# Kernel optimization log

Measured on AMD Instinct MI355X. Metric: run time of the kernel, lower is better.

Reference implementation:

```python
import jax, jax.numpy as jnp
import numpy as np

TOP_K = 8
N_EXPERTS = 64
ALPHA = 0.01

def setup_inputs() -> dict:
    key = jax.random.key(0)
    k1, k2 = jax.random.split(key)
    hidden_states = jax.random.normal(k1, (8, 4096, 1024), dtype=jnp.float32)
    weight = jax.random.normal(k2, (N_EXPERTS, 1024), dtype=jnp.float32) * 0.02
    return {"hidden_states": hidden_states, "weight": weight}

def reference(hidden_states, weight):
    bsz, seq_len, h = hidden_states.shape
    tokens = hidden_states.reshape(-1, h).astype(jnp.float32)          # [T, h]
    logits = tokens @ weight.astype(jnp.float32).T                     # [T, E]
    scores = jax.nn.softmax(logits, axis=-1)                           # [T, E]
    topk_weights, topk_indices = jax.lax.top_k(scores, TOP_K)          # [T, K]
    topk_indices = jnp.clip(topk_indices, 0, N_EXPERTS - 1)
    # renormalize top-k probabilities (norm_topk_prob=True, top_k>1)
    denom = topk_weights.sum(axis=-1, keepdims=True) + 1e-20
    topk_weights = topk_weights / denom
    # expert usage counts (bincount / scatter path)
    expert_counts = jnp.zeros((N_EXPERTS,), jnp.int32).at[topk_indices.reshape(-1)].add(1)
    # sequence aux loss (training path, seq_aux=True)
    idx_b = topk_indices.reshape(bsz, seq_len * TOP_K)                 # [B, S*K]
    ce = jnp.zeros((bsz, N_EXPERTS), jnp.float32)
    ce = ce.at[jnp.arange(bsz)[:, None], idx_b].add(1.0)
    ce = ce * (N_EXPERTS / (seq_len * TOP_K))
    scores_seq = scores.reshape(bsz, seq_len, N_EXPERTS)
    aux_loss = ((ce * scores_seq.mean(axis=1)).sum(axis=1)).mean() * ALPHA
    return (topk_indices.astype(jnp.int32),
            topk_weights.astype(hidden_states.dtype),
            aux_loss,
            expert_counts)
```

## Files before the change

kernel.cpp:

```cpp
#include <hip/hip_runtime.h>

#define NTOK 32768
#define HDIM 1024
#define NEXP 64
#define TK   8
#define NB   8
#define SEQ  4096

#define MB   64
#define KC   64
#define NCH  (HDIM / KC)
#define NTHR 512

typedef __attribute__((ext_vector_type(8))) short bf16x8;
typedef __attribute__((ext_vector_type(4))) float f32x4;

union BF8 { bf16x8 v; unsigned u[4]; };

__device__ inline unsigned f2bf(float x) {
    unsigned u = __float_as_uint(x);
    return (u + 0x7FFFu + ((u >> 16) & 1u)) >> 16;
}

__device__ inline void split4(float4 v, unsigned* hp, unsigned* lp) {
    unsigned h0 = f2bf(v.x), h1 = f2bf(v.y), h2 = f2bf(v.z), h3 = f2bf(v.w);
    unsigned l0 = f2bf(v.x - __uint_as_float(h0 << 16));
    unsigned l1 = f2bf(v.y - __uint_as_float(h1 << 16));
    unsigned l2 = f2bf(v.z - __uint_as_float(h2 << 16));
    unsigned l3 = f2bf(v.w - __uint_as_float(h3 << 16));
    hp[0] = h0 | (h1 << 16); hp[1] = h2 | (h3 << 16);
    lp[0] = l0 | (l1 << 16); lp[1] = l2 | (l3 << 16);
}

__device__ __forceinline__ void gl16(const void* g, void* l) {
    __builtin_amdgcn_global_load_lds(
        (const __attribute__((address_space(1))) void*)g,
        (__attribute__((address_space(3))) void*)l, 16, 0, 0);
}

__global__ void wsplit(const float* __restrict__ w,
                       unsigned short* __restrict__ whi,
                       unsigned short* __restrict__ wlo)
{
    int T = blockIdx.x * 256 + threadIdx.x;
    int slot = T >> 6, l = T & 63;
    int c = slot >> 3, s = (slot >> 2) & 1, n = slot & 3;
    int e = n * 16 + (l & 15);
    int k = c * 64 + s * 32 + (l >> 4) * 8;
    const float* src = w + (size_t)e * HDIM + k;
    float4 v0 = *(const float4*)(src);
    float4 v1 = *(const float4*)(src + 4);
    unsigned hp[4], lp[4];
    split4(v0, &hp[0], &lp[0]);
    split4(v1, &hp[2], &lp[2]);
    ((uint4*)whi)[T] = make_uint4(hp[0], hp[1], hp[2], hp[3]);
    ((uint4*)wlo)[T] = make_uint4(lp[0], lp[1], lp[2], lp[3]);
}

__global__ __launch_bounds__(NTHR, 4) void moe_main(
    const float* __restrict__ hidden,
    const unsigned short* __restrict__ w2hi,
    const unsigned short* __restrict__ w2lo,
    float* __restrict__ out,
    float* __restrict__ ws)
{
    __shared__ __align__(16) unsigned char smem[32768];
    float* sLog = (float*)smem;
    __shared__ float mxArr[MB];
    __shared__ float smSum[NEXP];
    __shared__ int   hist[NEXP];

    const int tid   = threadIdx.x;
    const int w     = tid >> 6;
    const int l     = tid & 63;
    const int m     = l & 15;
    const int q     = l >> 4;
    const int wm    = w >> 1;
    const int wn    = w & 1;
    const int t0    = blockIdx.x * MB;
    const int wbase = tid & 448;

    if (tid < NEXP) { smSum[tid] = 0.f; hist[tid] = 0; }

    f32x4 acc[2];
#pragma unroll
    for (int n = 0; n < 2; ++n) acc[n] = (f32x4)0.f;

#pragma unroll
    for (int i = 0; i < 2; ++i) {
        int slot = i * NTHR + tid;
        int r = slot >> 4, p = slot & 15, b = p ^ (r & 15);
        gl16(hidden + (size_t)(t0 + r) * HDIM + b * 4,
             smem + (size_t)(i * NTHR + wbase) * 16);
    }
    __syncthreads();

    for (int c = 0; c < NCH; ++c) {
        const unsigned char* Ab = smem + (c & 1) * 16384;

        bf16x8 bh[2][2], bl[2][2];
#pragma unroll
        for (int s = 0; s < 2; ++s)
#pragma unroll
            for (int n = 0; n < 2; ++n) {
                size_t off = ((size_t)(c * 8 + s * 4 + wn * 2 + n) * 64 + l) * 8;
                bh[s][n] = *(const bf16x8*)(w2hi + off);
                bl[s][n] = *(const bf16x8*)(w2lo + off);
            }

        if (c + 1 < NCH) {
            unsigned char* nb = smem + ((c + 1) & 1) * 16384;
            const int kc = (c + 1) * KC;
#pragma unroll
            for (int i = 0; i < 2; ++i) {
                int slot = i * NTHR + tid;
                int r = slot >> 4, p = slot & 15, b = p ^ (r & 15);
                gl16(hidden + (size_t)(t0 + r) * HDIM + kc + b * 4,
                     nb + (size_t)(i * NTHR + wbase) * 16);
            }
        }

#pragma unroll
        for (int s = 0; s < 2; ++s) {
            const int r  = wm * 16 + m;
            const int b0 = s * 8 + q * 2;
            const int p0 = b0 ^ m, p1 = (b0 + 1) ^ m;
            float4 a0 = *(const float4*)(Ab + ((size_t)r * 16 + p0) * 16);
            float4 a1 = *(const float4*)(Ab + ((size_t)r * 16 + p1) * 16);
            BF8 ah, al;
            split4(a0, &ah.u[0], &al.u[0]);
            split4(a1, &ah.u[2], &al.u[2]);
#pragma unroll
            for (int n = 0; n < 2; ++n) {
                acc[n] = __builtin_amdgcn_mfma_f32_16x16x32_bf16(ah.v, bh[s][n], acc[n], 0, 0, 0);
                acc[n] = __builtin_amdgcn_mfma_f32_16x16x32_bf16(al.v, bh[s][n], acc[n], 0, 0, 0);
                acc[n] = __builtin_amdgcn_mfma_f32_16x16x32_bf16(ah.v, bl[s][n], acc[n], 0, 0, 0);
            }
        }
        __syncthreads();
    }

#pragma unroll
    for (int n = 0; n < 2; ++n)
#pragma unroll
        for (int r = 0; r < 4; ++r)
            sLog[(wm * 16 + q * 4 + r) * 66 + (wn * 2 + n) * 16 + m] = acc[n][r];
    __syncthreads();

    float regSm = 0.f;
    for (int j = 0; j < 8; ++j) {
        int t = w * 8 + j;
        float x = sLog[t * 66 + l];
        float mx = x;
#pragma unroll
        for (int off = 32; off; off >>= 1) mx = fmaxf(mx, __shfl_xor(mx, off));
        float p = __expf(x - mx);
        float sd = p;
#pragma unroll
        for (int off = 32; off; off >>= 1) sd += __shfl_xor(sd, off);
        regSm += p / sd;
        if (l == 0) mxArr[t] = mx;
    }
    atomicAdd(&smSum[l], regSm);
    __syncthreads();

    if (w == 0) {
        const float mx = mxArr[l];
        unsigned long long s8[TK];
#pragma unroll
        for (int j = 0; j < TK; ++j) s8[j] = 0ull;
        for (int e = 0; e < NEXP; ++e) {
            float x = sLog[l * 66 + e];
            unsigned u = __float_as_uint(x);
            unsigned k32 = (u & 0x80000000u) ? ~u : (u | 0x80000000u);
            unsigned long long key = ((unsigned long long)k32 << 6)
                                   | (unsigned long long)(63 - e);
            if (key > s8[TK - 1]) {
#pragma unroll
                for (int j = 0; j < TK; ++j) {
                    unsigned long long hi = s8[j] > key ? s8[j] : key;
                    key = s8[j] > key ? key : s8[j];
                    s8[j] = hi;
                }
            }
        }
        float ev[TK]; int ei[TK]; float sum = 0.f;
#pragma unroll
        for (int j = 0; j < TK; ++j) {
            unsigned k32 = (unsigned)(s8[j] >> 6);
            unsigned u = (k32 >> 31) ? (k32 ^ 0x80000000u) : ~k32;
            ev[j] = __expf(__uint_as_float(u) - mx);
            sum += ev[j];
            ei[j] = 63 - (int)(s8[j] & 63ull);
        }
        int t = t0 + l;
        float4 i0 = make_float4((float)ei[0], (float)ei[1], (float)ei[2], (float)ei[3]);
        float4 i1 = make_float4((float)ei[4], (float)ei[5], (float)ei[6], (float)ei[7]);
        *(float4*)(out + (size_t)t * TK)     = i0;
        *(float4*)(out + (size_t)t * TK + 4) = i1;
        float rs = 1.f / (sum + 1e-20f);
        float4 w0 = make_float4(ev[0] * rs, ev[1] * rs, ev[2] * rs, ev[3] * rs);
        float4 w1 = make_float4(ev[4] * rs, ev[5] * rs, ev[6] * rs, ev[7] * rs);
        *(float4*)(out + (size_t)NTOK * TK + (size_t)t * TK)     = w0;
        *(float4*)(out + (size_t)NTOK * TK + (size_t)t * TK + 4) = w1;
#pragma unroll
        for (int j = 0; j < TK; ++j) atomicAdd(&hist[ei[j]], 1);
    }
    __syncthreads();

    if (tid < NEXP) {
        int b = blockIdx.x >> 6;
        atomicAdd(&ws[b * NEXP + tid], (float)hist[tid]);
        atomicAdd(&ws[NB * NEXP + b * NEXP + tid], smSum[tid]);
    }
}

__global__ void moe_finalize(const float* __restrict__ ws, float* __restrict__ out)
{
    int e = threadIdx.x;
    float cnt = 0.f, accv = 0.f;
#pragma unroll
    for (int b = 0; b < NB; ++b) {
        float c  = ws[b * NEXP + e];
        float sm = ws[NB * NEXP + b * NEXP + e];
        cnt += c;
        accv += c * sm;
    }
    out[(size_t)NTOK * TK * 2 + 1 + e] = cnt;
#pragma unroll
    for (int off = 32; off; off >>= 1) accv += __shfl_xor(accv, off);
    if (e == 0) {
        float aux = 0.01f * accv * ((float)NEXP / ((float)SEQ * (float)TK))
                    / (float)SEQ / (float)NB;
        out[(size_t)NTOK * TK * 2] = aux;
    }
}

extern "C" void kernel_launch(void* const* d_in, const int* in_sizes, int n_in,
                              void* d_out, int out_size, void* d_ws, size_t ws_size,
                              hipStream_t stream)
{
    const float* hidden = (const float*)d_in[0];
    const float* weight = (const float*)d_in[1];
    float* out  = (float*)d_out;
    float* wsf  = (float*)d_ws;
    unsigned short* w2hi = (unsigned short*)(wsf + 2 * NB * NEXP);
    unsigned short* w2lo = w2hi + NEXP * HDIM;

    hipMemsetAsync(d_ws, 0, 2 * NB * NEXP * sizeof(float), stream);
    wsplit<<<32, 256, 0, stream>>>(weight, w2hi, w2lo);
    moe_main<<<NTOK / MB, NTHR, 0, stream>>>(hidden, w2hi, w2lo, out, wsf);
    moe_finalize<<<1, 64, 0, stream>>>(wsf, out);
}
```

Baseline: 231.8 us.

## Restructure GEMM into 16-token full-K tiles with double-buffered LDS prefetch

Each block now handles 128 tokens as 8 sequential 16-token tiles. Every tile loads the full 1024-wide hidden rows (64KB) into double-buffered LDS, and each of 4 waves computes 16 experts over the whole K dimension. Softmax and top-k run per tile, spread across waves. The goal is to overlap the next tile's load with the current tile's compute and cut per-chunk synchronisation. The cost is 128KB of LDS per block, which limits occupancy to about one block per CU. Weight fragments are also reloaded from global memory for every tile.

```diff
diff --git a/kernel.cpp b/kernel.cpp
--- a/kernel.cpp
+++ b/kernel.cpp
@@ -7,10 +7,13 @@
 #define NB   8
 #define SEQ  4096
 
-#define MB   64
-#define KC   64
-#define NCH  (HDIM / KC)
-#define NTHR 512
+#define TPB   128
+#define TT    16
+#define NTILE (TPB / TT)
+#define NTHR  256
+#define NBLK  (NTOK / TPB)
+
+#define ABUF  65536
 
 typedef __attribute__((ext_vector_type(8))) short bf16x8;
 typedef __attribute__((ext_vector_type(4))) float f32x4;
@@ -57,16 +60,15 @@
     ((uint4*)wlo)[T] = make_uint4(lp[0], lp[1], lp[2], lp[3]);
 }
 
-__global__ __launch_bounds__(NTHR, 4) void moe_main(
+__global__ __launch_bounds__(NTHR, 1) void moe_main(
     const float* __restrict__ hidden,
     const unsigned short* __restrict__ w2hi,
     const unsigned short* __restrict__ w2lo,
     float* __restrict__ out,
     float* __restrict__ ws)
 {
-    __shared__ __align__(16) unsigned char smem[32768];
-    float* sLog = (float*)smem;
-    __shared__ float mxArr[MB];
+    __shared__ __align__(16) unsigned char smem[2 * ABUF];
+    __shared__ float sLog[TT * 66];
     __shared__ float smSum[NEXP];
     __shared__ int   hist[NEXP];
 
@@ -75,141 +77,135 @@
     const int l     = tid & 63;
     const int m     = l & 15;
     const int q     = l >> 4;
-    const int wm    = w >> 1;
-    const int wn    = w & 1;
-    const int t0    = blockIdx.x * MB;
-    const int wbase = tid & 448;
+    const int wbase = tid & 192;
+    const size_t t0 = (size_t)blockIdx.x * TPB;
 
     if (tid < NEXP) { smSum[tid] = 0.f; hist[tid] = 0; }
 
-    f32x4 acc[2];
-#pragma unroll
-    for (int n = 0; n < 2; ++n) acc[n] = (f32x4)0.f;
-
-#pragma unroll
-    for (int i = 0; i < 2; ++i) {
-        int slot = i * NTHR + tid;
-        int r = slot >> 4, p = slot & 15, b = p ^ (r & 15);
-        gl16(hidden + (size_t)(t0 + r) * HDIM + b * 4,
-             smem + (size_t)(i * NTHR + wbase) * 16);
+    {
+        const float* base = hidden + t0 * HDIM;
+#pragma unroll
+        for (int i = 0; i < 16; ++i) {
+            int L = i * NTHR + tid;
+            int r = L >> 8;
+            int u = L & 255;
+            int sc = (u & 0xF0) | ((u & 15) ^ r);
+            gl16(base + (size_t)r * HDIM + sc * 4,
+                 smem + (size_t)(i * NTHR + wbase) * 16);
+        }
     }
     __syncthreads();
 
-    for (int c = 0; c < NCH; ++c) {
-        const unsigned char* Ab = smem + (c & 1) * 16384;
-
-        bf16x8 bh[2][2], bl[2][2];
-#pragma unroll
-        for (int s = 0; s < 2; ++s)
-#pragma unroll
-            for (int n = 0; n < 2; ++n) {
-                size_t off = ((size_t)(c * 8 + s * 4 + wn * 2 + n) * 64 + l) * 8;
-                bh[s][n] = *(const bf16x8*)(w2hi + off);
-                bl[s][n] = *(const bf16x8*)(w2lo + off);
-            }
-
-        if (c + 1 < NCH) {
-            unsigned char* nb = smem + ((c + 1) & 1) * 16384;
-            const int kc = (c + 1) * KC;
-#pragma unroll
-            for (int i = 0; i < 2; ++i) {
-                int slot = i * NTHR + tid;
-                int r = slot >> 4, p = slot & 15, b = p ^ (r & 15);
-                gl16(hidden + (size_t)(t0 + r) * HDIM + kc + b * 4,
+    float mxKeep = 0.f;
+
+    for (int tile = 0; tile < NTILE; ++tile) {
+        const unsigned char* Ab = smem + (tile & 1) * ABUF;
+
+        if (tile + 1 < NTILE) {
+            unsigned char* nb = smem + ((tile + 1) & 1) * ABUF;
+            const float* base = hidden + (t0 + (size_t)(tile + 1) * TT) * HDIM;
+#pragma unroll
+            for (int i = 0; i < 16; ++i) {
+                int L = i * NTHR + tid;
+                int r = L >> 8;
+                int u = L & 255;
+                int sc = (u & 0xF0) | ((u & 15) ^ r);
+                gl16(base + (size_t)r * HDIM + sc * 4,
                      nb + (size_t)(i * NTHR + wbase) * 16);
             }
         }
 
-#pragma unroll
-        for (int s = 0; s < 2; ++s) {
-            const int r  = wm * 16 + m;
-            const int b0 = s * 8 + q * 2;
-            const int p0 = b0 ^ m, p1 = (b0 + 1) ^ m;
-            float4 a0 = *(const float4*)(Ab + ((size_t)r * 16 + p0) * 16);
-            float4 a1 = *(const float4*)(Ab + ((size_t)r * 16 + p1) * 16);
+        f32x4 acc = (f32x4)0.f;
+#pragma unroll
+        for (int s = 0; s < 32; ++s) {
+            size_t boff = ((size_t)((s >> 1) * 8 + (s & 1) * 4 + w) * 64 + l) * 8;
+            bf16x8 bh = *(const bf16x8*)(w2hi + boff);
+            bf16x8 bl = *(const bf16x8*)(w2lo + boff);
+            int grp = (s >> 1) << 4;
+            int p0  = ((s & 1) * 8 + q * 2)     ^ m;
+            int p1  = ((s & 1) * 8 + q * 2 + 1) ^ m;
+            float4 a0 = *(const float4*)(Ab + ((size_t)(m << 8) + grp + p0) * 16);
+            float4 a1 = *(const float4*)(Ab + ((size_t)(m << 8) + grp + p1) * 16);
             BF8 ah, al;
             split4(a0, &ah.u[0], &al.u[0]);
             split4(a1, &ah.u[2], &al.u[2]);
-#pragma unroll
-            for (int n = 0; n < 2; ++n) {
-                acc[n] = __builtin_amdgcn_mfma_f32_16x16x32_bf16(ah.v, bh[s][n], acc[n], 0, 0, 0);
-                acc[n] = __builtin_amdgcn_mfma_f32_16x16x32_bf16(al.v, bh[s][n], acc[n], 0, 0, 0);
-                acc[n] = __builtin_amdgcn_mfma_f32_16x16x32_bf16(ah.v, bl[s][n], acc[n], 0, 0, 0);
-            }
-        }
+            acc = __builtin_amdgcn_mfma_f32_16x16x32_bf16(ah.v, bh, acc, 0, 0, 0);
+            acc = __builtin_amdgcn_mfma_f32_16x16x32_bf16(al.v, bh, acc, 0, 0, 0);
+            acc = __builtin_amdgcn_mfma_f32_16x16x32_bf16(ah.v, bl, acc, 0, 0, 0);
+        }
+
         __syncthreads();
-    }
-
-#pragma unroll
-    for (int n = 0; n < 2; ++n)
-#pragma unroll
-        for (int r = 0; r < 4; ++r)
-            sLog[(wm * 16 + q * 4 + r) * 66 + (wn * 2 + n) * 16 + m] = acc[n][r];
-    __syncthreads();
-
-    float regSm = 0.f;
-    for (int j = 0; j < 8; ++j) {
-        int t = w * 8 + j;
-        float x = sLog[t * 66 + l];
-        float mx = x;
-#pragma unroll
-        for (int off = 32; off; off >>= 1) mx = fmaxf(mx, __shfl_xor(mx, off));
-        float p = __expf(x - mx);
-        float sd = p;
-#pragma unroll
-        for (int off = 32; off; off >>= 1) sd += __shfl_xor(sd, off);
-        regSm += p / sd;
-        if (l == 0) mxArr[t] = mx;
-    }
-    atomicAdd(&smSum[l], regSm);
-    __syncthreads();
-
-    if (w == 0) {
-        const float mx = mxArr[l];
-        unsigned long long s8[TK];
-#pragma unroll
-        for (int j = 0; j < TK; ++j) s8[j] = 0ull;
-        for (int e = 0; e < NEXP; ++e) {
-            float x = sLog[l * 66 + e];
-            unsigned u = __float_as_uint(x);
-            unsigned k32 = (u & 0x80000000u) ? ~u : (u | 0x80000000u);
-            unsigned long long key = ((unsigned long long)k32 << 6)
-                                   | (unsigned long long)(63 - e);
-            if (key > s8[TK - 1]) {
-#pragma unroll
-                for (int j = 0; j < TK; ++j) {
-                    unsigned long long hi = s8[j] > key ? s8[j] : key;
-                    key = s8[j] > key ? key : s8[j];
-                    s8[j] = hi;
+
+#pragma unroll
+        for (int rr = 0; rr < 4; ++rr)
+            sLog[(q * 4 + rr) * 66 + w * 16 + m] = acc[rr];
+        __syncthreads();
+
+        float regSm = 0.f;
+#pragma unroll
+        for (int jj = 0; jj < 4; ++jj) {
+            int t = w * 4 + jj;
+            float x = sLog[t * 66 + l];
+            float mx = x;
+#pragma unroll
+            for (int off = 32; off; off >>= 1) mx = fmaxf(mx, __shfl_xor(mx, off));
+            float p = __expf(x - mx);
+            float sd = p;
+#pragma unroll
+            for (int off = 32; off; off >>= 1) sd += __shfl_xor(sd, off);
+            regSm += p / sd;
+            if (jj == (l & 3)) mxKeep = mx;
+        }
+        atomicAdd(&smSum[l], regSm);
+
+        if (l < 4) {
+            const int   tl = w * 4 + l;
+            const float mx = mxKeep;
+            unsigned long long s8[TK];
+#pragma unroll
+            for (int j = 0; j < TK; ++j) s8[j] = 0ull;
+            for (int e = 0; e < NEXP; ++e) {
+                float x = sLog[tl * 66 + e];
+                unsigned u = __float_as_uint(x);
+                unsigned k32 = (u & 0x80000000u) ? ~u : (u | 0x80000000u);
+                unsigned long long key = ((unsigned long long)k32 << 6)
+                                       | (unsigned long long)(63 - e);
+                if (key > s8[TK - 1]) {
+#pragma unroll
+                    for (int j = 0; j < TK; ++j) {
+                        unsigned long long hi = s8[j] > key ? s8[j] : key;
+                        key = s8[j] > key ? key : s8[j];
+                        s8[j] = hi;
+                    }
                 }
             }
-        }
-        float ev[TK]; int ei[TK]; float sum = 0.f;
-#pragma unroll
-        for (int j = 0; j < TK; ++j) {
-            unsigned k32 = (unsigned)(s8[j] >> 6);
-            unsigned u = (k32 >> 31) ? (k32 ^ 0x80000000u) : ~k32;
-            ev[j] = __expf(__uint_as_float(u) - mx);
-            sum += ev[j];
-            ei[j] = 63 - (int)(s8[j] & 63ull);
-        }
-        int t = t0 + l;
-        float4 i0 = make_float4((float)ei[0], (float)ei[1], (float)ei[2], (float)ei[3]);
-        float4 i1 = make_float4((float)ei[4], (float)ei[5], (float)ei[6], (float)ei[7]);
-        *(float4*)(out + (size_t)t * TK)     = i0;
-        *(float4*)(out + (size_t)t * TK + 4) = i1;
-        float rs = 1.f / (sum + 1e-20f);
-        float4 w0 = make_float4(ev[0] * rs, ev[1] * rs, ev[2] * rs, ev[3] * rs);
-        float4 w1 = make_float4(ev[4] * rs, ev[5] * rs, ev[6] * rs, ev[7] * rs);
-        *(float4*)(out + (size_t)NTOK * TK + (size_t)t * TK)     = w0;
-        *(float4*)(out + (size_t)NTOK * TK + (size_t)t * TK + 4) = w1;
-#pragma unroll
-        for (int j = 0; j < TK; ++j) atomicAdd(&hist[ei[j]], 1);
+            float ev[TK]; int ei[TK]; float sum = 0.f;
+#pragma unroll
+            for (int j = 0; j < TK; ++j) {
+                unsigned k32 = (unsigned)(s8[j] >> 6);
+                unsigned u = (k32 >> 31) ? (k32 ^ 0x80000000u) : ~k32;
+                ev[j] = __expf(__uint_as_float(u) - mx);
+                sum += ev[j];
+                ei[j] = 63 - (int)(s8[j] & 63ull);
+            }
+            size_t t = t0 + (size_t)tile * TT + tl;
+            float4 i0 = make_float4((float)ei[0], (float)ei[1], (float)ei[2], (float)ei[3]);
+            float4 i1 = make_float4((float)ei[4], (float)ei[5], (float)ei[6], (float)ei[7]);
+            *(float4*)(out + t * TK)     = i0;
+            *(float4*)(out + t * TK + 4) = i1;
+            float rs = 1.f / (sum + 1e-20f);
+            float4 w0 = make_float4(ev[0] * rs, ev[1] * rs, ev[2] * rs, ev[3] * rs);
+            float4 w1 = make_float4(ev[4] * rs, ev[5] * rs, ev[6] * rs, ev[7] * rs);
+            *(float4*)(out + (size_t)NTOK * TK + t * TK)     = w0;
+            *(float4*)(out + (size_t)NTOK * TK + t * TK + 4) = w1;
+#pragma unroll
+            for (int j = 0; j < TK; ++j) atomicAdd(&hist[ei[j]], 1);
+        }
     }
     __syncthreads();
 
     if (tid < NEXP) {
-        int b = blockIdx.x >> 6;
+        int b = blockIdx.x >> 5;
         atomicAdd(&ws[b * NEXP + tid], (float)hist[tid]);
         atomicAdd(&ws[NB * NEXP + b * NEXP + tid], smSum[tid]);
     }
@@ -249,6 +245,6 @@
 
     hipMemsetAsync(d_ws, 0, 2 * NB * NEXP * sizeof(float), stream);
     wsplit<<<32, 256, 0, stream>>>(weight, w2hi, w2lo);
-    moe_main<<<NTOK / MB, NTHR, 0, stream>>>(hidden, w2hi, w2lo, out, wsf);
+    moe_main<<<NBLK, NTHR, 0, stream>>>(hidden, w2hi, w2lo, out, wsf);
     moe_finalize<<<1, 64, 0, stream>>>(wsf, out);
 }
```

New measurement: 399.7 us. 1.72x slower.

## Split GEMM from gating and add 5-deep async ring buffer for hidden and weights

Applied to the files above, without the earlier changes.

Splits the fused kernel into a GEMM kernel that writes logits to workspace and a separate gating kernel for softmax, top-k and aux stats. The GEMM now uses 128-token tiles with K-chunks of 32, stages both the hidden-state slice and the weight hi/lo slices through a 5-slot LDS ring with prefetch three chunks ahead, and waits with explicit vmcnt counts instead of a full __syncthreads per chunk. The goal is to hide global-load latency on the memory-bound hidden-state stream and to reuse the weight fragments across two M sub-tiles. In exchange the logits make an extra round trip through global memory, there is one more kernel launch, and occupancy drops because of the larger LDS footprint.

```diff
diff --git a/kernel.cpp b/kernel.cpp
--- a/kernel.cpp
+++ b/kernel.cpp
@@ -7,10 +7,16 @@
 #define NB   8
 #define SEQ  4096
 
-#define MB   64
-#define KC   64
-#define NCH  (HDIM / KC)
-#define NTHR 512
+#define MB    128
+#define KC    32
+#define NCH   (HDIM / KC)
+#define NTHR  512
+#define NBLK  (NTOK / MB)
+
+#define RING  5
+#define CH_A  16384
+#define CH_B  4096
+#define CHSZ  (CH_A + 2 * CH_B)
 
 typedef __attribute__((ext_vector_type(8))) short bf16x8;
 typedef __attribute__((ext_vector_type(4))) float f32x4;
@@ -57,18 +63,13 @@
     ((uint4*)wlo)[T] = make_uint4(lp[0], lp[1], lp[2], lp[3]);
 }
 
-__global__ __launch_bounds__(NTHR, 4) void moe_main(
+__global__ __launch_bounds__(NTHR, 2) void moe_gemm(
     const float* __restrict__ hidden,
     const unsigned short* __restrict__ w2hi,
     const unsigned short* __restrict__ w2lo,
-    float* __restrict__ out,
-    float* __restrict__ ws)
-{
-    __shared__ __align__(16) unsigned char smem[32768];
-    float* sLog = (float*)smem;
-    __shared__ float mxArr[MB];
-    __shared__ float smSum[NEXP];
-    __shared__ int   hist[NEXP];
+    float* __restrict__ logits)
+{
+    __shared__ __align__(16) unsigned char smem[RING * CHSZ];
 
     const int tid   = threadIdx.x;
     const int w     = tid >> 6;
@@ -77,76 +78,118 @@
     const int q     = l >> 4;
     const int wm    = w >> 1;
     const int wn    = w & 1;
-    const int t0    = blockIdx.x * MB;
     const int wbase = tid & 448;
-
-    if (tid < NEXP) { smSum[tid] = 0.f; hist[tid] = 0; }
-
-    f32x4 acc[2];
-#pragma unroll
-    for (int n = 0; n < 2; ++n) acc[n] = (f32x4)0.f;
-
-#pragma unroll
-    for (int i = 0; i < 2; ++i) {
-        int slot = i * NTHR + tid;
-        int r = slot >> 4, p = slot & 15, b = p ^ (r & 15);
-        gl16(hidden + (size_t)(t0 + r) * HDIM + b * 4,
-             smem + (size_t)(i * NTHR + wbase) * 16);
-    }
-    __syncthreads();
-
-    for (int c = 0; c < NCH; ++c) {
-        const unsigned char* Ab = smem + (c & 1) * 16384;
-
-        bf16x8 bh[2][2], bl[2][2];
-#pragma unroll
-        for (int s = 0; s < 2; ++s)
-#pragma unroll
-            for (int n = 0; n < 2; ++n) {
-                size_t off = ((size_t)(c * 8 + s * 4 + wn * 2 + n) * 64 + l) * 8;
-                bh[s][n] = *(const bf16x8*)(w2hi + off);
-                bl[s][n] = *(const bf16x8*)(w2lo + off);
-            }
-
-        if (c + 1 < NCH) {
-            unsigned char* nb = smem + ((c + 1) & 1) * 16384;
-            const int kc = (c + 1) * KC;
-#pragma unroll
-            for (int i = 0; i < 2; ++i) {
-                int slot = i * NTHR + tid;
-                int r = slot >> 4, p = slot & 15, b = p ^ (r & 15);
-                gl16(hidden + (size_t)(t0 + r) * HDIM + kc + b * 4,
-                     nb + (size_t)(i * NTHR + wbase) * 16);
-            }
-        }
-
-#pragma unroll
-        for (int s = 0; s < 2; ++s) {
-            const int r  = wm * 16 + m;
-            const int b0 = s * 8 + q * 2;
-            const int p0 = b0 ^ m, p1 = (b0 + 1) ^ m;
-            float4 a0 = *(const float4*)(Ab + ((size_t)r * 16 + p0) * 16);
-            float4 a1 = *(const float4*)(Ab + ((size_t)r * 16 + p1) * 16);
+    const size_t t0 = (size_t)blockIdx.x * MB;
+
+    const unsigned short* bsrc = (w < 4) ? w2hi : w2lo;
+    const int w4   = w & 3;
+    const int bDst = CH_A + (w >> 2) * CH_B + w4 * 1024;
+
+    auto stage = [&](int kk, unsigned char* nb) {
+#pragma unroll
+        for (int i = 0; i < 2; ++i) {
+            int g  = i * NTHR + tid;
+            int r  = g >> 3;
+            int sp = (g & 7) ^ (r & 7);
+            gl16(hidden + (t0 + r) * HDIM + kk * KC + sp * 4,
+                 nb + (size_t)(i * NTHR + wbase) * 16);
+        }
+        gl16(bsrc + (size_t)kk * 2048 + (size_t)(w4 * 64 + l) * 8,
+             nb + bDst);
+    };
+
+    f32x4 acc[2][2];
+#pragma unroll
+    for (int mt = 0; mt < 2; ++mt)
+#pragma unroll
+        for (int n = 0; n < 2; ++n) acc[mt][n] = (f32x4)0.f;
+
+    stage(0, smem);
+    stage(1, smem + CHSZ);
+    stage(2, smem + 2 * CHSZ);
+
+    int bufR = 0, bufW = 3;
+    for (int kk = 0; kk < NCH; ++kk) {
+        if (kk + 3 < NCH) {
+            stage(kk + 3, smem + bufW * CHSZ);
+            bufW = (bufW == RING - 1) ? 0 : bufW + 1;
+        }
+        if      (kk + 3 <  NCH) asm volatile("s_waitcnt vmcnt(9)" ::: "memory");
+        else if (kk + 3 == NCH) asm volatile("s_waitcnt vmcnt(6)" ::: "memory");
+        else if (kk + 2 == NCH) asm volatile("s_waitcnt vmcnt(3)" ::: "memory");
+        else                    asm volatile("s_waitcnt vmcnt(0)" ::: "memory");
+        __builtin_amdgcn_s_barrier();
+        __builtin_amdgcn_sched_barrier(0);
+
+        const unsigned char* Ab = smem + bufR * CHSZ;
+        bufR = (bufR == RING - 1) ? 0 : bufR + 1;
+
+        bf16x8 bh[2], bl[2];
+#pragma unroll
+        for (int n = 0; n < 2; ++n) {
+            int off = CH_A + (wn * 2 + n) * 1024 + l * 16;
+            bh[n] = *(const bf16x8*)(Ab + off);
+            bl[n] = *(const bf16x8*)(Ab + CH_B + off);
+        }
+
+#pragma unroll
+        for (int mt = 0; mt < 2; ++mt) {
+            int r   = wm * 32 + mt * 16 + m;
+            int sp0 = (q * 2)     ^ (r & 7);
+            int sp1 = (q * 2 + 1) ^ (r & 7);
+            float4 a0 = *(const float4*)(Ab + ((size_t)r * 8 + sp0) * 16);
+            float4 a1 = *(const float4*)(Ab + ((size_t)r * 8 + sp1) * 16);
             BF8 ah, al;
             split4(a0, &ah.u[0], &al.u[0]);
             split4(a1, &ah.u[2], &al.u[2]);
 #pragma unroll
             for (int n = 0; n < 2; ++n) {
-                acc[n] = __builtin_amdgcn_mfma_f32_16x16x32_bf16(ah.v, bh[s][n], acc[n], 0, 0, 0);
-                acc[n] = __builtin_amdgcn_mfma_f32_16x16x32_bf16(al.v, bh[s][n], acc[n], 0, 0, 0);
-                acc[n] = __builtin_amdgcn_mfma_f32_16x16x32_bf16(ah.v, bl[s][n], acc[n], 0, 0, 0);
+                acc[mt][n] = __builtin_amdgcn_mfma_f32_16x16x32_bf16(ah.v, bh[n], acc[mt][n], 0, 0, 0);
+                acc[mt][n] = __builtin_amdgcn_mfma_f32_16x16x32_bf16(al.v, bh[n], acc[mt][n], 0, 0, 0);
+                acc[mt][n] = __builtin_amdgcn_mfma_f32_16x16x32_bf16(ah.v, bl[n], acc[mt][n], 0, 0, 0);
             }
         }
-        __syncthreads();
-    }
-
-#pragma unroll
-    for (int n = 0; n < 2; ++n)
-#pragma unroll
-        for (int r = 0; r < 4; ++r)
-            sLog[(wm * 16 + q * 4 + r) * 66 + (wn * 2 + n) * 16 + m] = acc[n][r];
+    }
+
+#pragma unroll
+    for (int mt = 0; mt < 2; ++mt)
+#pragma unroll
+        for (int n = 0; n < 2; ++n)
+#pragma unroll
+            for (int r = 0; r < 4; ++r)
+                logits[(t0 + wm * 32 + mt * 16 + q * 4 + r) * NEXP
+                       + wn * 32 + n * 16 + m] = acc[mt][n][r];
+}
+
+__global__ __launch_bounds__(512, 4) void moe_gate(
+    const float* __restrict__ logits,
+    float* __restrict__ out,
+    float* __restrict__ ws)
+{
+    __shared__ float sLog[64 * 66];
+    __shared__ float mxArr[64];
+    __shared__ float smSum[NEXP];
+    __shared__ int   hist[NEXP];
+
+    const int tid = threadIdx.x;
+    const int w   = tid >> 6;
+    const int l   = tid & 63;
+    const int t0  = blockIdx.x * 64;
+
+    if (tid < NEXP) { smSum[tid] = 0.f; hist[tid] = 0; }
+
+    const float4* src = (const float4*)(logits + (size_t)t0 * NEXP);
+#pragma unroll
+    for (int j = 0; j < 2; ++j) {
+        int g = j * 512 + tid;
+        float4 v = src[g];
+        int r = g >> 4, c = (g & 15) * 4;
+        float* d = &sLog[r * 66 + c];
+        d[0] = v.x; d[1] = v.y; d[2] = v.z; d[3] = v.w;
+    }
     __syncthreads();
 
+    float mxKeep = 0.f;
     float regSm = 0.f;
     for (int j = 0; j < 8; ++j) {
         int t = w * 8 + j;
@@ -160,6 +203,7 @@
         for (int off = 32; off; off >>= 1) sd += __shfl_xor(sd, off);
         regSm += p / sd;
         if (l == 0) mxArr[t] = mx;
+        (void)mxKeep;
     }
     atomicAdd(&smSum[l], regSm);
     __syncthreads();
@@ -246,9 +290,11 @@
     float* wsf  = (float*)d_ws;
     unsigned short* w2hi = (unsigned short*)(wsf + 2 * NB * NEXP);
     unsigned short* w2lo = w2hi + NEXP * HDIM;
+    float* logits = (float*)(w2lo + NEXP * HDIM);
 
     hipMemsetAsync(d_ws, 0, 2 * NB * NEXP * sizeof(float), stream);
     wsplit<<<32, 256, 0, stream>>>(weight, w2hi, w2lo);
-    moe_main<<<NTOK / MB, NTHR, 0, stream>>>(hidden, w2hi, w2lo, out, wsf);
+    moe_gemm<<<NBLK, NTHR, 0, stream>>>(hidden, w2hi, w2lo, logits);
+    moe_gate<<<NTOK / 64, 512, 0, stream>>>(logits, out, wsf);
     moe_finalize<<<1, 64, 0, stream>>>(wsf, out);
 }
```

After: 235.0 us. No clear change (+1.4%).
